# Performance work log

Measured on AMD Instinct MI355X. Metric: run time of the kernel, lower is better.

The kernel has to match this reference:

```python
import jax, jax.numpy as jnp
import numpy as np

N_NODES = 50000
N_EDGES = 1600000
IN_C, HID_C, OUT_C = 256, 256, 10


def setup_inputs() -> dict:
    key = jax.random.key(0)
    ks = jax.random.split(key, 8)
    x = jax.random.normal(ks[0], (N_NODES, IN_C), dtype=jnp.float32)
    edge_index = jax.random.randint(ks[1], (2, N_EDGES), 0, N_NODES, dtype=jnp.int64)
    s1 = 1.0 / np.sqrt(IN_C)
    s2 = 1.0 / np.sqrt(HID_C)
    W1l = jax.random.normal(ks[2], (IN_C, HID_C), dtype=jnp.float32) * s1
    W1r = jax.random.normal(ks[3], (IN_C, HID_C), dtype=jnp.float32) * s1
    b1 = jnp.zeros((HID_C,), dtype=jnp.float32)
    W2l = jax.random.normal(ks[4], (HID_C, OUT_C), dtype=jnp.float32) * s2
    W2r = jax.random.normal(ks[5], (HID_C, OUT_C), dtype=jnp.float32) * s2
    b2 = jnp.zeros((OUT_C,), dtype=jnp.float32)
    return {"x": x, "edge_index": edge_index, "W1l": W1l, "W1r": W1r,
            "b1": b1, "W2l": W2l, "W2r": W2r, "b2": b2}


def _mean_agg(x, src, dst, n):
    # scatter-mean of source features into destination nodes
    summed = jax.ops.segment_sum(x[src], dst, num_segments=n)  # [N, C]
    cnt = jax.ops.segment_sum(jnp.ones_like(dst, dtype=x.dtype), dst, num_segments=n)
    return summed / jnp.maximum(cnt, 1.0)[:, None]


def _sage_conv(x, src, dst, Wl, Wr, b):
    # PyG SAGEConv (mean aggr): lin_l(mean_j x_j) + lin_r(x_i) + bias
    n = x.shape[0]
    agg = _mean_agg(x, src, dst, n)
    return agg @ Wl + x @ Wr + b


def reference(x, edge_index, W1l, W1r, b1, W2l, W2r, b2):
    src = edge_index[0]
    dst = edge_index[1]
    h = _sage_conv(x, src, dst, W1l, W1r, b1)
    h = jax.nn.relu(h)  # dropout skipped: eval mode
    out = _sage_conv(h, src, dst, W2l, W2r, b2)
    return jax.nn.log_softmax(out, axis=1)
```

## Files before the change

### kernel.cpp

```cpp
#include <hip/hip_runtime.h>
#include <hip/hip_bf16.h>

#define N_NODES 50000
#define N_EDGES 1600000
#define IN_C 256
#define HID_C 256
#define OUT_C 10
#define CD_STRIDE 32
#define SLOT_CAP 96
#define NBUCKET 196
#define EBUF_CAP 9216
#define M_TILES 391

typedef short bf16x8 __attribute__((ext_vector_type(8)));
typedef float f32x4 __attribute__((ext_vector_type(4)));

static __device__ __forceinline__ float b2f(short v) {
    unsigned u = (unsigned)(unsigned short)v << 16;
    return __builtin_bit_cast(float, u);
}
static __device__ __forceinline__ short f2b(float f) {
    __hip_bfloat16 h = __float2bfloat16(f);
    return __builtin_bit_cast(short, h);
}
static __device__ __forceinline__ int4 pack8(float4 a, float4 b) {
    bf16x8 o;
    o[0] = f2b(a.x); o[1] = f2b(a.y); o[2] = f2b(a.z); o[3] = f2b(a.w);
    o[4] = f2b(b.x); o[5] = f2b(b.y); o[6] = f2b(b.z); o[7] = f2b(b.w);
    return __builtin_bit_cast(int4, o);
}

__global__ __launch_bounds__(256) void k_part(const int* __restrict__ src,
                                              const int* __restrict__ dst,
                                              int* __restrict__ g_cursor,
                                              int* __restrict__ ebuf) {
    __shared__ int hist[NBUCKET];
    __shared__ int base[NBUCKET];
    __shared__ int pos[NBUCKET];
    int tid = threadIdx.x;
    if (tid < NBUCKET) { hist[tid] = 0; pos[tid] = 0; }
    __syncthreads();

    int4 s[4], d[4];
    bool valid[4];
#pragma unroll
    for (int q = 0; q < 4; ++q) {
        int idx = blockIdx.x * 1024 + q * 256 + tid;
        valid[q] = (idx < N_EDGES / 4);
        if (valid[q]) {
            s[q] = ((const int4*)src)[idx];
            d[q] = ((const int4*)dst)[idx];
        }
    }
#pragma unroll
    for (int q = 0; q < 4; ++q) {
        if (valid[q]) {
            atomicAdd(&hist[d[q].x >> 8], 1);
            atomicAdd(&hist[d[q].y >> 8], 1);
            atomicAdd(&hist[d[q].z >> 8], 1);
            atomicAdd(&hist[d[q].w >> 8], 1);
        }
    }
    __syncthreads();
    if (tid < NBUCKET && hist[tid] > 0)
        base[tid] = atomicAdd(&g_cursor[tid], hist[tid]);
    __syncthreads();
#pragma unroll
    for (int q = 0; q < 4; ++q) {
        if (valid[q]) {
            int ss[4] = { s[q].x, s[q].y, s[q].z, s[q].w };
            int dd[4] = { d[q].x, d[q].y, d[q].z, d[q].w };
#pragma unroll
            for (int e = 0; e < 4; ++e) {
                int b = dd[e] >> 8;
                int p = base[b] + atomicAdd(&pos[b], 1);
                if (p < EBUF_CAP)
                    ebuf[b * EBUF_CAP + p] = ss[e] | ((dd[e] & 255) << 16);
            }
        }
    }
}

__global__ __launch_bounds__(256) void k_bucket(const int* __restrict__ ebuf,
                                                const int* __restrict__ g_cursor,
                                                int* __restrict__ cnt,
                                                unsigned short* __restrict__ slots) {
    __shared__ int lcnt[256];
    int b = blockIdx.x, tid = threadIdx.x;
    lcnt[tid] = 0;
    __syncthreads();
    int n_e = g_cursor[b];
    if (n_e > EBUF_CAP) n_e = EBUF_CAP;
    const int* eb = ebuf + b * EBUF_CAP;
    int n4 = n_e >> 2;
    for (int t = tid; t < n4; t += 256) {
        int4 v = ((const int4*)eb)[t];
        int vv[4] = { v.x, v.y, v.z, v.w };
#pragma unroll
        for (int e = 0; e < 4; ++e) {
            int dl = (vv[e] >> 16) & 255;
            int sv = vv[e] & 0xFFFF;
            int p = atomicAdd(&lcnt[dl], 1);
            if (p < SLOT_CAP) slots[(size_t)(b * 256 + dl) * SLOT_CAP + p] = (unsigned short)sv;
        }
    }
    for (int t = (n4 << 2) + tid; t < n_e; t += 256) {
        int vv = eb[t];
        int dl = (vv >> 16) & 255;
        int sv = vv & 0xFFFF;
        int p = atomicAdd(&lcnt[dl], 1);
        if (p < SLOT_CAP) slots[(size_t)(b * 256 + dl) * SLOT_CAP + p] = (unsigned short)sv;
    }
    __syncthreads();
    int nid = b * 256 + tid;
    if (nid < N_NODES) cnt[nid] = lcnt[tid];
}

__global__ void k_prep_w(const float* __restrict__ W1l, const float* __restrict__ W1r,
                         __hip_bfloat16* __restrict__ Wt) {
    int idx = blockIdx.x * 256 + threadIdx.x;
    int n = idx >> 8, k = idx & 255;
    float v = (n < HID_C) ? W1l[k * HID_C + n] : W1r[k * HID_C + (n - HID_C)];
    Wt[idx] = __float2bfloat16(v);
}

__global__ void k_prep_w2f(const float* __restrict__ W2l, const float* __restrict__ W2r,
                           float* __restrict__ Wt2f) {
    int idx = blockIdx.x * 256 + threadIdx.x;
    int r = idx >> 8, k = idx & 255;
    if (r < OUT_C) Wt2f[r * 256 + k] = W2l[k * OUT_C + r];
    else           Wt2f[(16 + r - OUT_C) * 256 + k] = W2r[k * OUT_C + (r - OUT_C)];
}

__global__ __launch_bounds__(256) void k_gemm1(
        const float* __restrict__ X, const __hip_bfloat16* __restrict__ Wt,
        const float* __restrict__ b1,
        __hip_bfloat16* __restrict__ Ab, __hip_bfloat16* __restrict__ Bh) {
    __shared__ short Smem[2 * 128 * 64];
    short* As = Smem;
    short* Bs = Smem + 128 * 64;
    int fid = blockIdx.x;
    int xcd = fid & 7, slot = fid >> 3;
    int m_t = (slot >> 2) * 8 + xcd;
    if (m_t >= M_TILES) return;
    int n_t = slot & 3;
    int m_base = m_t * 128;
    int n_base = n_t * 128;

    int tid = threadIdx.x;
    int wave = tid >> 6, lane = tid & 63;
    int r = lane & 15, quad = lane >> 4;
    int wr = wave >> 1, wc = wave & 1;

    int srow = tid >> 3;
    int kb8  = (tid & 7) * 16;
    int kelem = (tid & 7) * 8;
    int swz  = kb8 ^ ((srow & 7) << 4);

    f32x4 acc[4][4];
#pragma unroll
    for (int i = 0; i < 4; ++i)
#pragma unroll
        for (int j = 0; j < 4; ++j) acc[i][j] = f32x4{0.f, 0.f, 0.f, 0.f};

    int4 av[4], bv[4];
#pragma unroll
    for (int q = 0; q < 4; ++q) {
        int grow = m_base + q * 32 + srow;
        if (grow > N_NODES - 1) grow = N_NODES - 1;
        const float* xp = X + (size_t)grow * IN_C + kelem;
        av[q] = pack8(*(const float4*)xp, *(const float4*)(xp + 4));
        int brow = n_base + q * 32 + srow;
        bv[q] = *(const int4*)((const char*)Wt + ((size_t)brow * 512 + kb8));
    }

    for (int kk = 0; kk < 4; ++kk) {
        if (kk) __syncthreads();
#pragma unroll
        for (int q = 0; q < 4; ++q) {
            *(int4*)((char*)As + (size_t)((q * 32 + srow) * 128 + swz)) = av[q];
            *(int4*)((char*)Bs + (size_t)((q * 32 + srow) * 128 + swz)) = bv[q];
        }
        __syncthreads();

        if (kk < 3) {
            int ke = (kk + 1) * 64 + kelem;
            int kbyte = (kk + 1) * 128 + kb8;
#pragma unroll
            for (int q = 0; q < 4; ++q) {
                int grow = m_base + q * 32 + srow;
                if (grow > N_NODES - 1) grow = N_NODES - 1;
                const float* xp = X + (size_t)grow * IN_C + ke;
                av[q] = pack8(*(const float4*)xp, *(const float4*)(xp + 4));
                int brow = n_base + q * 32 + srow;
                bv[q] = *(const int4*)((const char*)Wt + ((size_t)brow * 512 + kbyte));
            }
        }

#pragma unroll
        for (int s = 0; s < 2; ++s) {
            int kfb = (s * 64 + quad * 16) ^ ((r & 7) << 4);
            bf16x8 a[4], b[4];
#pragma unroll
            for (int i = 0; i < 4; ++i)
                a[i] = *(const bf16x8*)((const char*)As + (size_t)((wr * 64 + i * 16 + r) * 128) + kfb);
#pragma unroll
            for (int j = 0; j < 4; ++j)
                b[j] = *(const bf16x8*)((const char*)Bs + (size_t)((wc * 64 + j * 16 + r) * 128) + kfb);
#pragma unroll
            for (int i = 0; i < 4; ++i)
#pragma unroll
                for (int j = 0; j < 4; ++j)
                    acc[i][j] = __builtin_amdgcn_mfma_f32_16x16x32_bf16(a[i], b[j], acc[i][j], 0, 0, 0);
        }
    }

    __syncthreads();
    short* Cs = Smem;
    bool left = (n_base < HID_C);
#pragma unroll
    for (int j = 0; j < 4; ++j) {
        int coll = wc * 64 + 16 * j + r;
        float bias = left ? 0.f : b1[n_base + coll - HID_C];
#pragma unroll
        for (int i = 0; i < 4; ++i) {
#pragma unroll
            for (int ii = 0; ii < 4; ++ii) {
                int rowl = wr * 64 + 16 * i + quad * 4 + ii;
                int byteoff = (coll * 2) ^ ((rowl & 7) << 4);
                *(short*)((char*)Cs + rowl * 256 + byteoff) = f2b(acc[i][j][ii] + bias);
            }
        }
    }
    __syncthreads();

    int rrow = tid >> 4;
    int cchunk = (tid & 15) * 16;
    size_t colbyte = left ? (size_t)(n_base * 2) : (size_t)((n_base - HID_C) * 2);
    char* outp = left ? (char*)Ab : (char*)Bh;
    for (int rb = 0; rb < 128; rb += 16) {
        int rowl = rb + rrow;
        int4 v = *(const int4*)((const char*)Cs + rowl * 256 + (cchunk ^ ((rowl & 7) << 4)));
        int grow = m_base + rowl;
        if (grow < N_NODES)
            *(int4*)(outp + (size_t)grow * 512 + colbyte + cchunk) = v;
    }
}

__global__ __launch_bounds__(256) void k_agg1f(
        const __hip_bfloat16* __restrict__ Ab, const __hip_bfloat16* __restrict__ Bh,
        const int* __restrict__ cnt, const unsigned short* __restrict__ slots,
        const float* __restrict__ Wt2f, const float* __restrict__ b2,
        float* __restrict__ CD) {
    int wave = threadIdx.x >> 6, lane = threadIdx.x & 63;
    int nid = blockIdx.x * 4 + wave;
    int half = lane >> 5;
    int c8 = (lane & 31) * 8;
    const unsigned short* row = slots + (size_t)nid * SLOT_CAP;
    int n = cnt[nid];
    if (n > SLOT_CAP) n = SLOT_CAP;
    int mid = (n + 1) >> 1;
    int beg = half ? mid : 0;
    int end = half ? n : mid;

    float s0[8], s1[8], s2[8], s3[8];
#pragma unroll
    for (int j = 0; j < 8; ++j) { s0[j] = 0.f; s1[j] = 0.f; s2[j] = 0.f; s3[j] = 0.f; }

    const __hip_bfloat16* abc = Ab + c8;
    int e = beg;
    for (; e + 8 <= end; e += 8) {
        int i0 = row[e],     i1 = row[e + 1], i2 = row[e + 2], i3 = row[e + 3];
        int i4 = row[e + 4], i5 = row[e + 5], i6 = row[e + 6], i7 = row[e + 7];
        bf16x8 v0 = *(const bf16x8*)(abc + (size_t)i0 * HID_C);
        bf16x8 v1 = *(const bf16x8*)(abc + (size_t)i1 * HID_C);
        bf16x8 v2 = *(const bf16x8*)(abc + (size_t)i2 * HID_C);
        bf16x8 v3 = *(const bf16x8*)(abc + (size_t)i3 * HID_C);
        bf16x8 v4 = *(const bf16x8*)(abc + (size_t)i4 * HID_C);
        bf16x8 v5 = *(const bf16x8*)(abc + (size_t)i5 * HID_C);
        bf16x8 v6 = *(const bf16x8*)(abc + (size_t)i6 * HID_C);
        bf16x8 v7 = *(const bf16x8*)(abc + (size_t)i7 * HID_C);
#pragma unroll
        for (int j = 0; j < 8; ++j) {
            s0[j] += b2f(v0[j]) + b2f(v4[j]);
            s1[j] += b2f(v1[j]) + b2f(v5[j]);
            s2[j] += b2f(v2[j]) + b2f(v6[j]);
            s3[j] += b2f(v3[j]) + b2f(v7[j]);
        }
    }
    for (; e + 4 <= end; e += 4) {
        int i0 = row[e], i1 = row[e + 1], i2 = row[e + 2], i3 = row[e + 3];
        bf16x8 v0 = *(const bf16x8*)(abc + (size_t)i0 * HID_C);
        bf16x8 v1 = *(const bf16x8*)(abc + (size_t)i1 * HID_C);
        bf16x8 v2 = *(const bf16x8*)(abc + (size_t)i2 * HID_C);
        bf16x8 v3 = *(const bf16x8*)(abc + (size_t)i3 * HID_C);
#pragma unroll
        for (int j = 0; j < 8; ++j) {
            s0[j] += b2f(v0[j]); s1[j] += b2f(v1[j]);
            s2[j] += b2f(v2[j]); s3[j] += b2f(v3[j]);
        }
    }
    for (; e < end; ++e) {
        int i0 = row[e];
        bf16x8 v0 = *(const bf16x8*)(abc + (size_t)i0 * HID_C);
#pragma unroll
        for (int j = 0; j < 8; ++j) s0[j] += b2f(v0[j]);
    }
#pragma unroll
    for (int j = 0; j < 8; ++j) s0[j] += (s1[j] + s2[j]) + s3[j];
#pragma unroll
    for (int j = 0; j < 8; ++j) s0[j] += __shfl_down(s0[j], 32, 64);

    float h[8];
    float inv = 1.f / fmaxf((float)n, 1.f);
    if (half == 0) {
        bf16x8 bb = *(const bf16x8*)(Bh + (size_t)nid * HID_C + c8);
#pragma unroll
        for (int j = 0; j < 8; ++j)
            h[j] = fmaxf(s0[j] * inv + b2f(bb[j]), 0.f);
    }
#pragma unroll
    for (int j = 0; j < 8; ++j) h[j] = __shfl(h[j], lane & 31, 64);

    const float* wbase = Wt2f + (half ? 16 * 256 : 0);
    float acc[10];
#pragma unroll
    for (int j = 0; j < 10; ++j) {
        f32x4 w0 = *(const f32x4*)(wbase + j * 256 + c8);
        f32x4 w1 = *(const f32x4*)(wbase + j * 256 + c8 + 4);
        float a = h[0] * w0[0] + h[1] * w0[1] + h[2] * w0[2] + h[3] * w0[3]
                + h[4] * w1[0] + h[5] * w1[1] + h[6] * w1[2] + h[7] * w1[3];
#pragma unroll
        for (int off = 16; off > 0; off >>= 1)
            a += __shfl_down(a, off, 32);
        acc[j] = a;
    }
    if ((lane & 31) == 0) {
        float* o = CD + (size_t)nid * CD_STRIDE + half * 16;
        if (half == 0) {
#pragma unroll
            for (int j = 0; j < 10; ++j) o[j] = acc[j];
            o[10] = 0.f; o[11] = 0.f;
        } else {
#pragma unroll
            for (int j = 0; j < 10; ++j) o[j] = acc[j] + b2[j];
        }
    }
}

__global__ __launch_bounds__(256) void k_agg2(
        const float* __restrict__ CD, const int* __restrict__ cnt,
        const unsigned short* __restrict__ slots, float* __restrict__ out) {
    int wave = threadIdx.x >> 6, lane = threadIdx.x & 63;
    int half = lane >> 5, sub = lane & 31;
    int nid = blockIdx.x * 8 + wave * 2 + half;
    const unsigned short* row = slots + (size_t)nid * SLOT_CAP;
    int n = cnt[nid];
    if (n > SLOT_CAP) n = SLOT_CAP;
    float s[10];
#pragma unroll
    for (int j = 0; j < 10; ++j) s[j] = 0.f;
    for (int e = sub; e < n; e += 32) {
        const float* cr = CD + (size_t)row[e] * CD_STRIDE;
        f32x4 v0 = *(const f32x4*)cr;
        f32x4 v1 = *(const f32x4*)(cr + 4);
        f32x4 v2 = *(const f32x4*)(cr + 8);
#pragma unroll
        for (int j = 0; j < 4; ++j) { s[j] += v0[j]; s[4 + j] += v1[j]; }
        s[8] += v2[0]; s[9] += v2[1];
    }
#pragma unroll
    for (int j = 0; j < 10; ++j)
#pragma unroll
        for (int off = 16; off > 0; off >>= 1)
            s[j] += __shfl_down(s[j], off, 32);
    if (sub == 0) {
        float inv = 1.f / fmaxf((float)n, 1.f);
        float z[10], mx = -1e30f;
#pragma unroll
        for (int j = 0; j < 10; ++j) {
            z[j] = s[j] * inv + CD[(size_t)nid * CD_STRIDE + 16 + j];
            mx = fmaxf(mx, z[j]);
        }
        float se = 0.f;
#pragma unroll
        for (int j = 0; j < 10; ++j) se += expf(z[j] - mx);
        float lse = logf(se) + mx;
#pragma unroll
        for (int j = 0; j < 10; ++j) out[(size_t)nid * OUT_C + j] = z[j] - lse;
    }
}

extern "C" void kernel_launch(void* const* d_in, const int* in_sizes, int n_in,
                              void* d_out, int out_size, void* d_ws, size_t ws_size,
                              hipStream_t stream) {
    const float* x   = (const float*)d_in[0];
    const int*   ei  = (const int*)d_in[1];
    const float* W1l = (const float*)d_in[2];
    const float* W1r = (const float*)d_in[3];
    const float* b1  = (const float*)d_in[4];
    const float* W2l = (const float*)d_in[5];
    const float* W2r = (const float*)d_in[6];
    const float* b2  = (const float*)d_in[7];
    float* out = (float*)d_out;
    const int* src = ei;
    const int* dst = ei + N_EDGES;

    char* w = (char*)d_ws;
    size_t off = 0;
    auto alloc = [&](size_t bytes) -> void* {
        void* p = w + off;
        off = (off + bytes + 255) & ~(size_t)255;
        return p;
    };
    __hip_bfloat16* Wt   = (__hip_bfloat16*)alloc((size_t)2 * HID_C * IN_C * 2);
    float*          Wt2f = (float*)alloc((size_t)32 * 256 * 4);
    __hip_bfloat16* Ab   = (__hip_bfloat16*)alloc((size_t)N_NODES * HID_C * 2);
    __hip_bfloat16* Bh   = (__hip_bfloat16*)alloc((size_t)N_NODES * HID_C * 2);
    float* CD = (float*)alloc((size_t)N_NODES * CD_STRIDE * 4);
    int* cnt      = (int*)alloc((size_t)N_NODES * 4);
    unsigned short* slots = (unsigned short*)alloc((size_t)N_NODES * SLOT_CAP * 2);
    int* g_cursor = (int*)alloc((size_t)NBUCKET * 4);
    int* ebuf     = (int*)alloc((size_t)NBUCKET * EBUF_CAP * 4);

    (void)hipMemsetAsync(g_cursor, 0, (size_t)NBUCKET * 4, stream);

    k_part<<<(N_EDGES / 4 + 1023) / 1024, 256, 0, stream>>>(src, dst, g_cursor, ebuf);
    k_bucket<<<NBUCKET, 256, 0, stream>>>(ebuf, g_cursor, cnt, slots);

    k_prep_w<<<512, 256, 0, stream>>>(W1l, W1r, Wt);
    k_prep_w2f<<<20, 256, 0, stream>>>(W2l, W2r, Wt2f);

    k_gemm1<<<8 * 196, 256, 0, stream>>>(x, Wt, b1, Ab, Bh);
    k_agg1f<<<N_NODES / 4, 256, 0, stream>>>(Ab, Bh, cnt, slots, Wt2f, b2, CD);
    k_agg2<<<N_NODES / 8, 256, 0, stream>>>(CD, cnt, slots, out);
}
```

Baseline: 327.0 us.

## Split layer-1 aggregation into column-chunked passes over a blocked feature layout

GEMM1 now writes the neighbour-projected features in a column-blocked layout: eight 32-column chunks, each stored as a contiguous [N_NODES, 32] bf16 array. A new gather kernel runs one pass per chunk, so each pass gathers from a 3.2 MB slice that can stay in cache instead of the whole 25.6 MB table. A separate epilogue kernel then applies the mean, residual, ReLU and the second-layer projection. This adds one kernel launch and an extra intermediate buffer that is written and read back. Each pass also re-reads the slot lists, eight times in total.

```diff
diff --git a/kernel.cpp b/kernel.cpp
--- a/kernel.cpp
+++ b/kernel.cpp
@@ -11,6 +11,7 @@
 #define NBUCKET 196
 #define EBUF_CAP 9216
 #define M_TILES 391
+#define NPASS 8
 
 typedef short bf16x8 __attribute__((ext_vector_type(8)));
 typedef float f32x4 __attribute__((ext_vector_type(4)));
@@ -135,7 +136,7 @@
 __global__ __launch_bounds__(256) void k_gemm1(
         const float* __restrict__ X, const __hip_bfloat16* __restrict__ Wt,
         const float* __restrict__ b1,
-        __hip_bfloat16* __restrict__ Ab, __hip_bfloat16* __restrict__ Bh) {
+        __hip_bfloat16* __restrict__ Ab2, __hip_bfloat16* __restrict__ Bh) {
     __shared__ short Smem[2 * 128 * 64];
     short* As = Smem;
     short* Bs = Smem + 128 * 64;
@@ -236,91 +237,97 @@
 
     int rrow = tid >> 4;
     int cchunk = (tid & 15) * 16;
-    size_t colbyte = left ? (size_t)(n_base * 2) : (size_t)((n_base - HID_C) * 2);
-    char* outp = left ? (char*)Ab : (char*)Bh;
     for (int rb = 0; rb < 128; rb += 16) {
         int rowl = rb + rrow;
         int4 v = *(const int4*)((const char*)Cs + rowl * 256 + (cchunk ^ ((rowl & 7) << 4)));
         int grow = m_base + rowl;
-        if (grow < N_NODES)
-            *(int4*)(outp + (size_t)grow * 512 + colbyte + cchunk) = v;
-    }
-}
-
-__global__ __launch_bounds__(256) void k_agg1f(
-        const __hip_bfloat16* __restrict__ Ab, const __hip_bfloat16* __restrict__ Bh,
-        const int* __restrict__ cnt, const unsigned short* __restrict__ slots,
+        if (grow < N_NODES) {
+            if (left) {
+                int c0 = n_base + (cchunk >> 1);
+                *(int4*)((char*)Ab2 + ((size_t)(c0 >> 5) * N_NODES + grow) * 64 + (c0 & 31) * 2) = v;
+            } else {
+                *(int4*)((char*)Bh + (size_t)grow * 512 + (size_t)((n_base - HID_C) * 2) + cchunk) = v;
+            }
+        }
+    }
+}
+
+__global__ __launch_bounds__(256) void k_aggc(
+        const __hip_bfloat16* __restrict__ Ab2,
+        const int* __restrict__ cnt,
+        const unsigned short* __restrict__ slots,
+        __hip_bfloat16* __restrict__ agg) {
+    int wave = threadIdx.x >> 6, lane = threadIdx.x & 63;
+    int pass = blockIdx.y;
+    int h = lane >> 5, g = (lane >> 2) & 7, c = lane & 3;
+    int nid = blockIdx.x * 8 + wave * 2 + h;
+    const unsigned short* row = slots + (size_t)nid * SLOT_CAP;
+    int n = cnt[nid];
+    if (n > SLOT_CAP) n = SLOT_CAP;
+
+    const char* base = (const char*)Ab2 + (size_t)pass * N_NODES * 64 + c * 16;
+
+    float a0 = 0.f, a1 = 0.f, a2 = 0.f, a3 = 0.f, a4 = 0.f, a5 = 0.f, a6 = 0.f, a7 = 0.f;
+    int e = 0;
+    for (; e + 16 <= n; e += 16) {
+        unsigned s0 = row[e + g], s1 = row[e + 8 + g];
+        int4 v0 = *(const int4*)(base + (size_t)(s0 * 64u));
+        int4 v1 = *(const int4*)(base + (size_t)(s1 * 64u));
+        bf16x8 b0 = __builtin_bit_cast(bf16x8, v0);
+        bf16x8 b1v = __builtin_bit_cast(bf16x8, v1);
+        a0 += b2f(b0[0]) + b2f(b1v[0]); a1 += b2f(b0[1]) + b2f(b1v[1]);
+        a2 += b2f(b0[2]) + b2f(b1v[2]); a3 += b2f(b0[3]) + b2f(b1v[3]);
+        a4 += b2f(b0[4]) + b2f(b1v[4]); a5 += b2f(b0[5]) + b2f(b1v[5]);
+        a6 += b2f(b0[6]) + b2f(b1v[6]); a7 += b2f(b0[7]) + b2f(b1v[7]);
+    }
+    if (e + 8 <= n) {
+        unsigned s0 = row[e + g];
+        int4 v0 = *(const int4*)(base + (size_t)(s0 * 64u));
+        bf16x8 b0 = __builtin_bit_cast(bf16x8, v0);
+        a0 += b2f(b0[0]); a1 += b2f(b0[1]); a2 += b2f(b0[2]); a3 += b2f(b0[3]);
+        a4 += b2f(b0[4]); a5 += b2f(b0[5]); a6 += b2f(b0[6]); a7 += b2f(b0[7]);
+        e += 8;
+    }
+    if (e + g < n) {
+        unsigned s0 = row[e + g];
+        int4 v0 = *(const int4*)(base + (size_t)(s0 * 64u));
+        bf16x8 b0 = __builtin_bit_cast(bf16x8, v0);
+        a0 += b2f(b0[0]); a1 += b2f(b0[1]); a2 += b2f(b0[2]); a3 += b2f(b0[3]);
+        a4 += b2f(b0[4]); a5 += b2f(b0[5]); a6 += b2f(b0[6]); a7 += b2f(b0[7]);
+    }
+#pragma unroll
+    for (int off = 4; off <= 16; off <<= 1) {
+        a0 += __shfl_xor(a0, off, 64); a1 += __shfl_xor(a1, off, 64);
+        a2 += __shfl_xor(a2, off, 64); a3 += __shfl_xor(a3, off, 64);
+        a4 += __shfl_xor(a4, off, 64); a5 += __shfl_xor(a5, off, 64);
+        a6 += __shfl_xor(a6, off, 64); a7 += __shfl_xor(a7, off, 64);
+    }
+    if (g == 0) {
+        float inv = 1.f / fmaxf((float)n, 1.f);
+        bf16x8 o;
+        o[0] = f2b(a0 * inv); o[1] = f2b(a1 * inv); o[2] = f2b(a2 * inv); o[3] = f2b(a3 * inv);
+        o[4] = f2b(a4 * inv); o[5] = f2b(a5 * inv); o[6] = f2b(a6 * inv); o[7] = f2b(a7 * inv);
+        *(int4*)((char*)agg + (size_t)pass * N_NODES * 64 + (size_t)nid * 64 + c * 16) =
+            __builtin_bit_cast(int4, o);
+    }
+}
+
+__global__ __launch_bounds__(256) void k_epi(
+        const __hip_bfloat16* __restrict__ agg, const __hip_bfloat16* __restrict__ Bh,
         const float* __restrict__ Wt2f, const float* __restrict__ b2,
         float* __restrict__ CD) {
     int wave = threadIdx.x >> 6, lane = threadIdx.x & 63;
     int nid = blockIdx.x * 4 + wave;
-    int half = lane >> 5;
-    int c8 = (lane & 31) * 8;
-    const unsigned short* row = slots + (size_t)nid * SLOT_CAP;
-    int n = cnt[nid];
-    if (n > SLOT_CAP) n = SLOT_CAP;
-    int mid = (n + 1) >> 1;
-    int beg = half ? mid : 0;
-    int end = half ? n : mid;
-
-    float s0[8], s1[8], s2[8], s3[8];
-#pragma unroll
-    for (int j = 0; j < 8; ++j) { s0[j] = 0.f; s1[j] = 0.f; s2[j] = 0.f; s3[j] = 0.f; }
-
-    const __hip_bfloat16* abc = Ab + c8;
-    int e = beg;
-    for (; e + 8 <= end; e += 8) {
-        int i0 = row[e],     i1 = row[e + 1], i2 = row[e + 2], i3 = row[e + 3];
-        int i4 = row[e + 4], i5 = row[e + 5], i6 = row[e + 6], i7 = row[e + 7];
-        bf16x8 v0 = *(const bf16x8*)(abc + (size_t)i0 * HID_C);
-        bf16x8 v1 = *(const bf16x8*)(abc + (size_t)i1 * HID_C);
-        bf16x8 v2 = *(const bf16x8*)(abc + (size_t)i2 * HID_C);
-        bf16x8 v3 = *(const bf16x8*)(abc + (size_t)i3 * HID_C);
-        bf16x8 v4 = *(const bf16x8*)(abc + (size_t)i4 * HID_C);
-        bf16x8 v5 = *(const bf16x8*)(abc + (size_t)i5 * HID_C);
-        bf16x8 v6 = *(const bf16x8*)(abc + (size_t)i6 * HID_C);
-        bf16x8 v7 = *(const bf16x8*)(abc + (size_t)i7 * HID_C);
-#pragma unroll
-        for (int j = 0; j < 8; ++j) {
-            s0[j] += b2f(v0[j]) + b2f(v4[j]);
-            s1[j] += b2f(v1[j]) + b2f(v5[j]);
-            s2[j] += b2f(v2[j]) + b2f(v6[j]);
-            s3[j] += b2f(v3[j]) + b2f(v7[j]);
-        }
-    }
-    for (; e + 4 <= end; e += 4) {
-        int i0 = row[e], i1 = row[e + 1], i2 = row[e + 2], i3 = row[e + 3];
-        bf16x8 v0 = *(const bf16x8*)(abc + (size_t)i0 * HID_C);
-        bf16x8 v1 = *(const bf16x8*)(abc + (size_t)i1 * HID_C);
-        bf16x8 v2 = *(const bf16x8*)(abc + (size_t)i2 * HID_C);
-        bf16x8 v3 = *(const bf16x8*)(abc + (size_t)i3 * HID_C);
-#pragma unroll
-        for (int j = 0; j < 8; ++j) {
-            s0[j] += b2f(v0[j]); s1[j] += b2f(v1[j]);
-            s2[j] += b2f(v2[j]); s3[j] += b2f(v3[j]);
-        }
-    }
-    for (; e < end; ++e) {
-        int i0 = row[e];
-        bf16x8 v0 = *(const bf16x8*)(abc + (size_t)i0 * HID_C);
-#pragma unroll
-        for (int j = 0; j < 8; ++j) s0[j] += b2f(v0[j]);
-    }
-#pragma unroll
-    for (int j = 0; j < 8; ++j) s0[j] += (s1[j] + s2[j]) + s3[j];
-#pragma unroll
-    for (int j = 0; j < 8; ++j) s0[j] += __shfl_down(s0[j], 32, 64);
-
+    int half = lane >> 5, sub = lane & 31;
+    int c8 = sub * 8;
+
+    bf16x8 mv = *(const bf16x8*)((const char*)agg +
+                 ((size_t)(sub >> 2) * N_NODES + nid) * 64 + (sub & 3) * 16);
+    bf16x8 bb = *(const bf16x8*)(Bh + (size_t)nid * HID_C + c8);
     float h[8];
-    float inv = 1.f / fmaxf((float)n, 1.f);
-    if (half == 0) {
-        bf16x8 bb = *(const bf16x8*)(Bh + (size_t)nid * HID_C + c8);
-#pragma unroll
-        for (int j = 0; j < 8; ++j)
-            h[j] = fmaxf(s0[j] * inv + b2f(bb[j]), 0.f);
-    }
-#pragma unroll
-    for (int j = 0; j < 8; ++j) h[j] = __shfl(h[j], lane & 31, 64);
+#pragma unroll
+    for (int j = 0; j < 8; ++j)
+        h[j] = fmaxf(b2f(mv[j]) + b2f(bb[j]), 0.f);
 
     const float* wbase = Wt2f + (half ? 16 * 256 : 0);
     float acc[10];
@@ -335,7 +342,7 @@
             a += __shfl_down(a, off, 32);
         acc[j] = a;
     }
-    if ((lane & 31) == 0) {
+    if (sub == 0) {
         float* o = CD + (size_t)nid * CD_STRIDE + half * 16;
         if (half == 0) {
 #pragma unroll
@@ -415,8 +422,9 @@
     };
     __hip_bfloat16* Wt   = (__hip_bfloat16*)alloc((size_t)2 * HID_C * IN_C * 2);
     float*          Wt2f = (float*)alloc((size_t)32 * 256 * 4);
-    __hip_bfloat16* Ab   = (__hip_bfloat16*)alloc((size_t)N_NODES * HID_C * 2);
+    __hip_bfloat16* Ab2  = (__hip_bfloat16*)alloc((size_t)N_NODES * HID_C * 2);
     __hip_bfloat16* Bh   = (__hip_bfloat16*)alloc((size_t)N_NODES * HID_C * 2);
+    __hip_bfloat16* agg  = (__hip_bfloat16*)alloc((size_t)N_NODES * HID_C * 2);
     float* CD = (float*)alloc((size_t)N_NODES * CD_STRIDE * 4);
     int* cnt      = (int*)alloc((size_t)N_NODES * 4);
     unsigned short* slots = (unsigned short*)alloc((size_t)N_NODES * SLOT_CAP * 2);
@@ -431,7 +439,8 @@
     k_prep_w<<<512, 256, 0, stream>>>(W1l, W1r, Wt);
     k_prep_w2f<<<20, 256, 0, stream>>>(W2l, W2r, Wt2f);
 
-    k_gemm1<<<8 * 196, 256, 0, stream>>>(x, Wt, b1, Ab, Bh);
-    k_agg1f<<<N_NODES / 4, 256, 0, stream>>>(Ab, Bh, cnt, slots, Wt2f, b2, CD);
+    k_gemm1<<<8 * 196, 256, 0, stream>>>(x, Wt, b1, Ab2, Bh);
+    k_aggc<<<dim3(N_NODES / 8, NPASS), 256, 0, stream>>>(Ab2, cnt, slots, agg);
+    k_epi<<<N_NODES / 4, 256, 0, stream>>>(agg, Bh, Wt2f, b2, CD);
     k_agg2<<<N_NODES / 8, 256, 0, stream>>>(CD, cnt, slots, out);
 }
```

New measurement: 351.8 us. 1.08x slower.

## Fuse edge partitioning into GEMM launch, merge weight prep, widen bucket kernel

Applied to the files above, without the earlier changes.

Edge partitioning and the first-layer GEMM now run as one launch, with the first 391 blocks doing the partition work and the rest doing GEMM tiles, so the memory-bound partition can overlap the compute-bound GEMM. The two weight-prep kernels are merged into a single launch, and the bucket kernel uses 512 threads per block. The 8-way unrolled gather loop in the first aggregation is removed, leaving the 4-way loop. Together these cut launch count and serialization, at the cost of heterogeneous blocks sharing one launch config and possibly less memory-level parallelism in the gather.

```diff
diff --git a/kernel.cpp b/kernel.cpp
--- a/kernel.cpp
+++ b/kernel.cpp
@@ -11,6 +11,7 @@
 #define NBUCKET 196
 #define EBUF_CAP 9216
 #define M_TILES 391
+#define PART_BLOCKS 391
 
 typedef short bf16x8 __attribute__((ext_vector_type(8)));
 typedef float f32x4 __attribute__((ext_vector_type(4)));
@@ -23,123 +24,90 @@
     __hip_bfloat16 h = __float2bfloat16(f);
     return __builtin_bit_cast(short, h);
 }
-static __device__ __forceinline__ int4 pack8(float4 a, float4 b) {
+static __device__ __forceinline__ int4 pack8i(float4 a, float4 b) {
     bf16x8 o;
     o[0] = f2b(a.x); o[1] = f2b(a.y); o[2] = f2b(a.z); o[3] = f2b(a.w);
     o[4] = f2b(b.x); o[5] = f2b(b.y); o[6] = f2b(b.z); o[7] = f2b(b.w);
     return __builtin_bit_cast(int4, o);
 }
 
-__global__ __launch_bounds__(256) void k_part(const int* __restrict__ src,
-                                              const int* __restrict__ dst,
-                                              int* __restrict__ g_cursor,
-                                              int* __restrict__ ebuf) {
-    __shared__ int hist[NBUCKET];
-    __shared__ int base[NBUCKET];
-    __shared__ int pos[NBUCKET];
-    int tid = threadIdx.x;
-    if (tid < NBUCKET) { hist[tid] = 0; pos[tid] = 0; }
-    __syncthreads();
-
-    int4 s[4], d[4];
-    bool valid[4];
-#pragma unroll
-    for (int q = 0; q < 4; ++q) {
-        int idx = blockIdx.x * 1024 + q * 256 + tid;
-        valid[q] = (idx < N_EDGES / 4);
-        if (valid[q]) {
-            s[q] = ((const int4*)src)[idx];
-            d[q] = ((const int4*)dst)[idx];
-        }
-    }
-#pragma unroll
-    for (int q = 0; q < 4; ++q) {
-        if (valid[q]) {
-            atomicAdd(&hist[d[q].x >> 8], 1);
-            atomicAdd(&hist[d[q].y >> 8], 1);
-            atomicAdd(&hist[d[q].z >> 8], 1);
-            atomicAdd(&hist[d[q].w >> 8], 1);
-        }
-    }
-    __syncthreads();
-    if (tid < NBUCKET && hist[tid] > 0)
-        base[tid] = atomicAdd(&g_cursor[tid], hist[tid]);
-    __syncthreads();
-#pragma unroll
-    for (int q = 0; q < 4; ++q) {
-        if (valid[q]) {
-            int ss[4] = { s[q].x, s[q].y, s[q].z, s[q].w };
-            int dd[4] = { d[q].x, d[q].y, d[q].z, d[q].w };
-#pragma unroll
-            for (int e = 0; e < 4; ++e) {
-                int b = dd[e] >> 8;
-                int p = base[b] + atomicAdd(&pos[b], 1);
-                if (p < EBUF_CAP)
-                    ebuf[b * EBUF_CAP + p] = ss[e] | ((dd[e] & 255) << 16);
-            }
-        }
-    }
-}
-
-__global__ __launch_bounds__(256) void k_bucket(const int* __restrict__ ebuf,
-                                                const int* __restrict__ g_cursor,
-                                                int* __restrict__ cnt,
-                                                unsigned short* __restrict__ slots) {
-    __shared__ int lcnt[256];
-    int b = blockIdx.x, tid = threadIdx.x;
-    lcnt[tid] = 0;
-    __syncthreads();
-    int n_e = g_cursor[b];
-    if (n_e > EBUF_CAP) n_e = EBUF_CAP;
-    const int* eb = ebuf + b * EBUF_CAP;
-    int n4 = n_e >> 2;
-    for (int t = tid; t < n4; t += 256) {
-        int4 v = ((const int4*)eb)[t];
-        int vv[4] = { v.x, v.y, v.z, v.w };
-#pragma unroll
-        for (int e = 0; e < 4; ++e) {
-            int dl = (vv[e] >> 16) & 255;
-            int sv = vv[e] & 0xFFFF;
-            int p = atomicAdd(&lcnt[dl], 1);
-            if (p < SLOT_CAP) slots[(size_t)(b * 256 + dl) * SLOT_CAP + p] = (unsigned short)sv;
-        }
-    }
-    for (int t = (n4 << 2) + tid; t < n_e; t += 256) {
-        int vv = eb[t];
-        int dl = (vv >> 16) & 255;
-        int sv = vv & 0xFFFF;
-        int p = atomicAdd(&lcnt[dl], 1);
-        if (p < SLOT_CAP) slots[(size_t)(b * 256 + dl) * SLOT_CAP + p] = (unsigned short)sv;
-    }
-    __syncthreads();
-    int nid = b * 256 + tid;
-    if (nid < N_NODES) cnt[nid] = lcnt[tid];
-}
-
-__global__ void k_prep_w(const float* __restrict__ W1l, const float* __restrict__ W1r,
-                         __hip_bfloat16* __restrict__ Wt) {
-    int idx = blockIdx.x * 256 + threadIdx.x;
-    int n = idx >> 8, k = idx & 255;
-    float v = (n < HID_C) ? W1l[k * HID_C + n] : W1r[k * HID_C + (n - HID_C)];
-    Wt[idx] = __float2bfloat16(v);
-}
-
-__global__ void k_prep_w2f(const float* __restrict__ W2l, const float* __restrict__ W2r,
-                           float* __restrict__ Wt2f) {
-    int idx = blockIdx.x * 256 + threadIdx.x;
-    int r = idx >> 8, k = idx & 255;
-    if (r < OUT_C) Wt2f[r * 256 + k] = W2l[k * OUT_C + r];
-    else           Wt2f[(16 + r - OUT_C) * 256 + k] = W2r[k * OUT_C + (r - OUT_C)];
-}
-
-__global__ __launch_bounds__(256) void k_gemm1(
+__global__ void k_prep(const float* __restrict__ W1l, const float* __restrict__ W1r,
+                       const float* __restrict__ W2l, const float* __restrict__ W2r,
+                       __hip_bfloat16* __restrict__ Wt, float* __restrict__ Wt2f) {
+    int bid = blockIdx.x;
+    if (bid < 512) {
+        int idx = bid * 256 + threadIdx.x;
+        int n = idx >> 8, k = idx & 255;
+        float v = (n < HID_C) ? W1l[k * HID_C + n] : W1r[k * HID_C + (n - HID_C)];
+        Wt[idx] = __float2bfloat16(v);
+    } else {
+        int idx = (bid - 512) * 256 + threadIdx.x;
+        int r = idx >> 8, k = idx & 255;
+        if (r < OUT_C) Wt2f[r * 256 + k] = W2l[k * OUT_C + r];
+        else           Wt2f[(16 + r - OUT_C) * 256 + k] = W2r[k * OUT_C + (r - OUT_C)];
+    }
+}
+
+__global__ __launch_bounds__(256) void k_gp(
+        const int* __restrict__ src, const int* __restrict__ dst,
+        int* __restrict__ g_cursor, int* __restrict__ ebuf,
         const float* __restrict__ X, const __hip_bfloat16* __restrict__ Wt,
         const float* __restrict__ b1,
         __hip_bfloat16* __restrict__ Ab, __hip_bfloat16* __restrict__ Bh) {
     __shared__ short Smem[2 * 128 * 64];
+    int tid = threadIdx.x;
+
+    if (blockIdx.x < PART_BLOCKS) {
+        int* hist = (int*)Smem;
+        int* base = hist + 256;
+        int* pos  = base + 256;
+        if (tid < NBUCKET) { hist[tid] = 0; pos[tid] = 0; }
+        __syncthreads();
+
+        int4 s[4], d[4];
+        bool valid[4];
+#pragma unroll
+        for (int q = 0; q < 4; ++q) {
+            int idx = blockIdx.x * 1024 + q * 256 + tid;
+            valid[q] = (idx < N_EDGES / 4);
+            if (valid[q]) {
+                s[q] = ((const int4*)src)[idx];
+                d[q] = ((const int4*)dst)[idx];
+            }
+        }
+#pragma unroll
+        for (int q = 0; q < 4; ++q) {
+            if (valid[q]) {
+                atomicAdd(&hist[d[q].x >> 8], 1);
+                atomicAdd(&hist[d[q].y >> 8], 1);
+                atomicAdd(&hist[d[q].z >> 8], 1);
+                atomicAdd(&hist[d[q].w >> 8], 1);
+            }
+        }
+        __syncthreads();
+        if (tid < NBUCKET && hist[tid] > 0)
+            base[tid] = atomicAdd(&g_cursor[tid], hist[tid]);
+        __syncthreads();
+#pragma unroll
+        for (int q = 0; q < 4; ++q) {
+            if (valid[q]) {
+                int ss[4] = { s[q].x, s[q].y, s[q].z, s[q].w };
+                int dd[4] = { d[q].x, d[q].y, d[q].z, d[q].w };
+#pragma unroll
+                for (int e = 0; e < 4; ++e) {
+                    int b = dd[e] >> 8;
+                    int p = base[b] + atomicAdd(&pos[b], 1);
+                    if (p < EBUF_CAP)
+                        ebuf[b * EBUF_CAP + p] = ss[e] | ((dd[e] & 255) << 16);
+                }
+            }
+        }
+        return;
+    }
+
     short* As = Smem;
     short* Bs = Smem + 128 * 64;
-    int fid = blockIdx.x;
+    int fid = blockIdx.x - PART_BLOCKS;
     int xcd = fid & 7, slot = fid >> 3;
     int m_t = (slot >> 2) * 8 + xcd;
     if (m_t >= M_TILES) return;
@@ -147,7 +115,6 @@
     int m_base = m_t * 128;
     int n_base = n_t * 128;
 
-    int tid = threadIdx.x;
     int wave = tid >> 6, lane = tid & 63;
     int r = lane & 15, quad = lane >> 4;
     int wr = wave >> 1, wc = wave & 1;
@@ -169,7 +136,7 @@
         int grow = m_base + q * 32 + srow;
         if (grow > N_NODES - 1) grow = N_NODES - 1;
         const float* xp = X + (size_t)grow * IN_C + kelem;
-        av[q] = pack8(*(const float4*)xp, *(const float4*)(xp + 4));
+        av[q] = pack8i(*(const float4*)xp, *(const float4*)(xp + 4));
         int brow = n_base + q * 32 + srow;
         bv[q] = *(const int4*)((const char*)Wt + ((size_t)brow * 512 + kb8));
     }
@@ -191,7 +158,7 @@
                 int grow = m_base + q * 32 + srow;
                 if (grow > N_NODES - 1) grow = N_NODES - 1;
                 const float* xp = X + (size_t)grow * IN_C + ke;
-                av[q] = pack8(*(const float4*)xp, *(const float4*)(xp + 4));
+                av[q] = pack8i(*(const float4*)xp, *(const float4*)(xp + 4));
                 int brow = n_base + q * 32 + srow;
                 bv[q] = *(const int4*)((const char*)Wt + ((size_t)brow * 512 + kbyte));
             }
@@ -244,6 +211,43 @@
         int grow = m_base + rowl;
         if (grow < N_NODES)
             *(int4*)(outp + (size_t)grow * 512 + colbyte + cchunk) = v;
+    }
+}
+
+__global__ __launch_bounds__(512) void k_bucket(const int* __restrict__ ebuf,
+                                                const int* __restrict__ g_cursor,
+                                                int* __restrict__ cnt,
+                                                unsigned short* __restrict__ slots) {
+    __shared__ int lcnt[256];
+    int b = blockIdx.x, tid = threadIdx.x;
+    if (tid < 256) lcnt[tid] = 0;
+    __syncthreads();
+    int n_e = g_cursor[b];
+    if (n_e > EBUF_CAP) n_e = EBUF_CAP;
+    const int* eb = ebuf + b * EBUF_CAP;
+    int n4 = n_e >> 2;
+    for (int t = tid; t < n4; t += 512) {
+        int4 v = ((const int4*)eb)[t];
+        int vv[4] = { v.x, v.y, v.z, v.w };
+#pragma unroll
+        for (int e = 0; e < 4; ++e) {
+            int dl = (vv[e] >> 16) & 255;
+            int sv = vv[e] & 0xFFFF;
+            int p = atomicAdd(&lcnt[dl], 1);
+            if (p < SLOT_CAP) slots[(size_t)(b * 256 + dl) * SLOT_CAP + p] = (unsigned short)sv;
+        }
+    }
+    for (int t = (n4 << 2) + tid; t < n_e; t += 512) {
+        int vv = eb[t];
+        int dl = (vv >> 16) & 255;
+        int sv = vv & 0xFFFF;
+        int p = atomicAdd(&lcnt[dl], 1);
+        if (p < SLOT_CAP) slots[(size_t)(b * 256 + dl) * SLOT_CAP + p] = (unsigned short)sv;
+    }
+    __syncthreads();
+    if (tid < 256) {
+        int nid = b * 256 + tid;
+        if (nid < N_NODES) cnt[nid] = lcnt[tid];
     }
 }
 
@@ -269,25 +273,6 @@
 
     const __hip_bfloat16* abc = Ab + c8;
     int e = beg;
-    for (; e + 8 <= end; e += 8) {
-        int i0 = row[e],     i1 = row[e + 1], i2 = row[e + 2], i3 = row[e + 3];
-        int i4 = row[e + 4], i5 = row[e + 5], i6 = row[e + 6], i7 = row[e + 7];
-        bf16x8 v0 = *(const bf16x8*)(abc + (size_t)i0 * HID_C);
-        bf16x8 v1 = *(const bf16x8*)(abc + (size_t)i1 * HID_C);
-        bf16x8 v2 = *(const bf16x8*)(abc + (size_t)i2 * HID_C);
-        bf16x8 v3 = *(const bf16x8*)(abc + (size_t)i3 * HID_C);
-        bf16x8 v4 = *(const bf16x8*)(abc + (size_t)i4 * HID_C);
-        bf16x8 v5 = *(const bf16x8*)(abc + (size_t)i5 * HID_C);
-        bf16x8 v6 = *(const bf16x8*)(abc + (size_t)i6 * HID_C);
-        bf16x8 v7 = *(const bf16x8*)(abc + (size_t)i7 * HID_C);
-#pragma unroll
-        for (int j = 0; j < 8; ++j) {
-            s0[j] += b2f(v0[j]) + b2f(v4[j]);
-            s1[j] += b2f(v1[j]) + b2f(v5[j]);
-            s2[j] += b2f(v2[j]) + b2f(v6[j]);
-            s3[j] += b2f(v3[j]) + b2f(v7[j]);
-        }
-    }
     for (; e + 4 <= end; e += 4) {
         int i0 = row[e], i1 = row[e + 1], i2 = row[e + 2], i3 = row[e + 3];
         bf16x8 v0 = *(const bf16x8*)(abc + (size_t)i0 * HID_C);
@@ -425,13 +410,10 @@
 
     (void)hipMemsetAsync(g_cursor, 0, (size_t)NBUCKET * 4, stream);
 
-    k_part<<<(N_EDGES / 4 + 1023) / 1024, 256, 0, stream>>>(src, dst, g_cursor, ebuf);
-    k_bucket<<<NBUCKET, 256, 0, stream>>>(ebuf, g_cursor, cnt, slots);
-
-    k_prep_w<<<512, 256, 0, stream>>>(W1l, W1r, Wt);
-    k_prep_w2f<<<20, 256, 0, stream>>>(W2l, W2r, Wt2f);
-
-    k_gemm1<<<8 * 196, 256, 0, stream>>>(x, Wt, b1, Ab, Bh);
+    k_prep<<<532, 256, 0, stream>>>(W1l, W1r, W2l, W2r, Wt, Wt2f);
+    k_gp<<<PART_BLOCKS + 8 * 196, 256, 0, stream>>>(src, dst, g_cursor, ebuf,
+                                                    x, Wt, b1, Ab, Bh);
+    k_bucket<<<NBUCKET, 512, 0, stream>>>(ebuf, g_cursor, cnt, slots);
     k_agg1f<<<N_NODES / 4, 256, 0, stream>>>(Ab, Bh, cnt, slots, Wt2f, b2, CD);
     k_agg2<<<N_NODES / 8, 256, 0, stream>>>(CD, cnt, slots, out);
 }
```

Measured after the change: 316.0 us. -3.4%, faster.
